# Performance work log

Hardware: AMD Instinct MI355X
Metric: run time of the kernel (lower is better)

The kernel has to match this reference:

```python
import jax, jax.numpy as jnp
import numpy as np

NUM_ITEMS = 50000
B = 512      # batch of (user, item) pairs
L = 50       # padded per-user item-list length
K = 20       # top_k: length of each context channel
H = 32       # hidden_dim
D = 32       # output_dim


def setup_inputs() -> dict:
    key = jax.random.key(0)
    ks = jax.random.split(key, 8)
    ctx = jax.random.normal(ks[0], (NUM_ITEMS, 10, K), dtype=jnp.float32)
    item_idxs = jax.random.randint(ks[1], (B,), 0, NUM_ITEMS)
    user_items = jax.random.randint(ks[2], (B, L), 0, NUM_ITEMS)
    user_lens = jax.random.randint(ks[3], (B,), 1, L + 1)  # ragged lengths in [1, L]
    W1 = jax.random.normal(ks[4], (5, 1, H), dtype=jnp.float32) * 0.1
    b1 = jnp.zeros((5, H), dtype=jnp.float32)
    W2 = jax.random.normal(ks[5], (5, H, D), dtype=jnp.float32) * 0.1
    b2 = jnp.zeros((5, D), dtype=jnp.float32)
    Wout = jax.random.normal(ks[6], (D, 1), dtype=jnp.float32) * 0.1
    bout = jnp.zeros((1,), dtype=jnp.float32)
    return dict(ctx=ctx, W1=W1, b1=b1, W2=W2, b2=b2, Wout=Wout, bout=bout,
                item_idxs=item_idxs, user_items=user_items, user_lens=user_lens)


def _item_rep(feat, W1, b1, W2, b2):
    """feat: [..., 10, K] context channels -> [..., 5*K, D] item representation.
    Channels (2c, 2c+1) go through com_{c+1}: a shared 1->H->D MLP applied to each
    scalar (unsqueeze(1) in the original), outputs of the two channels multiplied."""
    prefix = feat.shape[:-2]
    x = feat.reshape(prefix + (5, 2, K))                     # [..., 5, 2, K]
    w1 = W1[:, 0, :].reshape((5, 1, 1, H))                   # input_dim == 1
    h = jax.nn.relu(x[..., None] * w1 + b1.reshape((5, 1, 1, H)))   # [..., 5, 2, K, H]
    o = jnp.einsum('...cpkh,chd->...cpkd', h, W2) + b2.reshape((5, 1, 1, D))
    rep = o[..., 0, :, :] * o[..., 1, :, :]                  # [..., 5, K, D]
    return rep.reshape(prefix + (5 * K, D))


def reference(ctx, W1, b1, W2, b2, Wout, bout, item_idxs, user_items, user_lens):
    # Target-item representations: gather contexts then tiny MLPs. [B, 5K, D]
    item_rep = _item_rep(ctx[item_idxs], W1, b1, W2, b2)
    # Per-user item reps (padded ragged) and masked mean over the item list.
    u_rep = _item_rep(ctx[user_items], W1, b1, W2, b2)       # [B, L, 5K, D]
    mask = (jnp.arange(L)[None, :] < user_lens[:, None]).astype(u_rep.dtype)  # [B, L]
    u_mean = jnp.einsum('blnd,bl->bnd', u_rep, mask) / user_lens[:, None, None].astype(u_rep.dtype)
    inter = u_mean * item_rep                                # [B, 5K, D]
    pred = jax.nn.sigmoid(inter @ Wout + bout)               # [B, 5K, 1]
    return pred.reshape(B * 5 * K, 1)
```

## Files before the change

### kernel.cpp

```cpp
#include <hip/hip_runtime.h>
#include <math.h>

#define NITEMS 50000
#define BATCH  512
#define LLEN   50
#define KTOP   20
#define HDIM   32
#define DDIM   32
#define NCH    5
#define NSEG   33
#define NSCAL  200
#define NCELL  100
#define NCELLH 50
#define THRP   33
#define NWAVE  8
#define CSLOTH 7

typedef _Float16 h2 __attribute__((ext_vector_type(2)));

static __device__ __forceinline__ float dot2_acc(h2 a, h2 b, float c) {
#if __has_builtin(__builtin_amdgcn_fdot2)
    return __builtin_amdgcn_fdot2(a, b, c, false);
#else
    return fmaf((float)a.x, (float)b.x, fmaf((float)a.y, (float)b.y, c));
#endif
}

#define WS_THRS  0
#define WS_AB16  160
#define WS_ORDER 5440


__global__ __launch_bounds__(256) void cnn_setup(
        const float* __restrict__ W1, const float* __restrict__ b1,
        const float* __restrict__ W2, const float* __restrict__ b2,
        const int* __restrict__ user_lens,
        float* __restrict__ ws, int* __restrict__ order) {
    const int tid = threadIdx.x;

    if (blockIdx.x < NSEG) {
        __shared__ float sW1[NCH*HDIM], sB1[NCH*HDIM], sThr[NCH*HDIM];
        __shared__ int   sRank[NCH*HDIM];
        __shared__ float sW2[NCH*HDIM*DDIM];
        __shared__ float sB2[NCH*DDIM];

        for (int i = tid; i < NCH*HDIM; i += 256) { sW1[i] = W1[i]; sB1[i] = b1[i]; }
        for (int i = tid; i < NCH*HDIM*DDIM; i += 256) sW2[i] = W2[i];
        for (int i = tid; i < NCH*DDIM; i += 256) sB2[i] = b2[i];
        __syncthreads();

        for (int i = tid; i < NCH*HDIM; i += 256) {
            float w = sW1[i];
            sThr[i] = (w != 0.f) ? (-sB1[i] / w) : INFINITY;
        }
        __syncthreads();

        for (int i = tid; i < NCH*HDIM; i += 256) {
            int c = i / HDIM, h = i % HDIM;
            float thr = sThr[i];
            int rank = 0;
            for (int h2i = 0; h2i < HDIM; ++h2i) {
                float thr2 = sThr[c*HDIM + h2i];
                rank += (thr2 < thr || (thr2 == thr && h2i < h)) ? 1 : 0;
            }
            sRank[i] = rank;
            if (blockIdx.x == 0) ws[WS_THRS + c*HDIM + rank] = thr;
        }
        __syncthreads();

        const int s = blockIdx.x;
        if (tid < NCH*DDIM) {
            int c = tid / DDIM, d = tid % DDIM;
            float A = 0.f, Bv = 0.f;
#pragma unroll
            for (int h = 0; h < HDIM; ++h) {
                float w  = sW1[c*HDIM + h];
                float bb = sB1[c*HDIM + h];
                int   r  = sRank[c*HDIM + h];
                bool active = (w > 0.f) ? (r < s) : ((w < 0.f) ? (r >= s) : (bb > 0.f));
                if (active) {
                    float w2 = sW2[(c*HDIM + h)*DDIM + d];
                    A  = fmaf(w,  w2, A);
                    Bv = fmaf(bb, w2, Bv);
                }
            }
            Bv += sB2[c*DDIM + d];
            unsigned short* ab = (unsigned short*)(ws + WS_AB16);
            int d4 = d >> 2, dd = d & 3;
            int base = ((c*NSEG + s)*32 + d4*4)*2;
            _Float16 ah = (_Float16)A, bh = (_Float16)Bv;
            ab[base + 4*(dd>>1) + (dd&1)]     = __builtin_bit_cast(unsigned short, ah);
            ab[base + 4*(dd>>1) + 2 + (dd&1)] = __builtin_bit_cast(unsigned short, bh);
        }
    } else {
        __shared__ int sHist[LLEN + 1];
        for (int i = tid; i <= LLEN; i += 256) sHist[i] = 0;
        __syncthreads();
        for (int i = tid; i < BATCH; i += 256) atomicAdd(&sHist[user_lens[i]], 1);
        __syncthreads();
        if (tid == 0) {
            int accum = 0;
            for (int l = 1; l <= LLEN; ++l) { int c = sHist[l]; sHist[l] = accum; accum += c; }
        }
        __syncthreads();
        for (int i = tid; i < BATCH; i += 256) {
            int pos = atomicAdd(&sHist[user_lens[i]], 1);
            order[pos] = i;
        }
    }
}

__global__ __launch_bounds__(512, 8) void cnn_main(
        const float* __restrict__ ctx,  const float* __restrict__ ws,
        const float* __restrict__ Wout, const float* __restrict__ bout,
        const int* __restrict__ item_idxs, const int* __restrict__ user_items,
        const int* __restrict__ user_lens, const int* __restrict__ order,
        float* __restrict__ out) {
    __shared__ unsigned int sAB16[NCH*NSEG*32];
    __shared__ float  sThrS[NCH*THRP];
    __shared__ uint2  sxo[NWAVE][NCELLH];
    __shared__ uint2  sWt[NCELLH*8];
    __shared__ float  pRed[NWAVE][NCELLH];

    const int tid  = threadIdx.x;
    const int w    = tid >> 6;
    const int lane = tid & 63;
    const int g    = lane >> 3;
    const int d4   = lane & 7;

    const uint4* ABg = reinterpret_cast<const uint4*>(ws + WS_AB16);
    uint4* sAB4 = reinterpret_cast<uint4*>(sAB16);
    for (int i = tid; i < NCH*NSEG*8; i += 512) sAB4[i] = ABg[i];
    for (int i = tid; i < NCH*THRP; i += 512) {
        int c = i / THRP, j = i - c*THRP;
        sThrS[i] = (j < HDIM) ? ws[WS_THRS + c*HDIM + j] : 0.f;
    }

    const int rowSlot = blockIdx.x >> 1;
    const int half    = blockIdx.x & 1;
    const int rank = (rowSlot < 256) ? rowSlot : (767 - rowSlot);
    const int b    = order[rank];
    const int len  = user_lens[b];
    const float inv_len = 1.f / (float)len;
    const float bo = bout[0];
    const h2 wv0 = {(_Float16)Wout[4*d4],     (_Float16)Wout[4*d4 + 1]};
    const h2 wv1 = {(_Float16)Wout[4*d4 + 2], (_Float16)Wout[4*d4 + 3]};

    int sc[2], sdst[2], sgi[2];
#pragma unroll
    for (int r = 0; r < 2; ++r) {
        int lidx = lane + 64*r;
        int c    = lidx / 20, rr = lidx - c*20;
        int slot = rr / 10,  kk = rr - slot*10;
        sc[r]   = (lidx < 100) ? c : 0;
        sdst[r] = (c*10 + kk)*8 + slot*4;
        sgi[r]  = c*40 + slot*20 + half*10 + kk;
    }

    const int nstripe = (len > w) ? ((len - w + NWAVE - 1) / NWAVE) : 0;

    unsigned int wtA[CSLOTH], wtB[CSLOTH];
    float acc[CSLOTH];
#pragma unroll
    for (int i = 0; i < CSLOTH; ++i) acc[i] = 0.f;

    char* sxoB = (char*)&sxo[w][0];

    __syncthreads();

    float xp[2] = {0.f, 0.f};
    if (nstripe > 0) {
        const float* row = ctx + (size_t)user_items[b*LLEN + w] * NSCAL;
#pragma unroll
        for (int r = 0; r < 2; ++r) {
            int lidx = lane + 64*r;
            if (lidx < 100) xp[r] = row[sgi[r]];
        }
    }

    if (w == 0) {
        float xt[2] = {0.f, 0.f};
        const float* row = ctx + (size_t)item_idxs[b] * NSCAL;
#pragma unroll
        for (int r = 0; r < 2; ++r) {
            int lidx = lane + 64*r;
            if (lidx < 100) xt[r] = row[sgi[r]];
        }
#pragma unroll
        for (int r = 0; r < 2; ++r) {
            int lidx = lane + 64*r;
            if (lidx < 100) {
                float xv = xt[r];
                int base = sc[r]*THRP;
                int pos = 0;
                pos += (sThrS[base + pos + 15] < xv) ? 16 : 0;
                pos += (sThrS[base + pos + 7]  < xv) ? 8  : 0;
                pos += (sThrS[base + pos + 3]  < xv) ? 4  : 0;
                pos += (sThrS[base + pos + 1]  < xv) ? 2  : 0;
                pos += (sThrS[base + pos]      < xv) ? 1  : 0;
                unsigned int off = (unsigned int)((sc[r]*NSEG + pos) << 7);
                _Float16 xh = (_Float16)xv;
                unsigned int word = (unsigned int)__builtin_bit_cast(unsigned short, xh)
                                  | (off << 16);
                *(unsigned int*)(sxoB + sdst[r]) = word;
            }
        }
        __builtin_amdgcn_wave_barrier();
#pragma unroll
        for (int i = 0; i < CSLOTH; ++i) {
            int cell = g + 8*i;
            if (cell < NCELLH) {
                uint2 xo = sxo[0][cell];
                const uint4* p0 = (const uint4*)((const char*)sAB16 + (xo.x >> 16) + (d4 << 4));
                const uint4* p1 = (const uint4*)((const char*)sAB16 + (xo.y >> 16) + (d4 << 4));
                uint4 q0 = *p0, q1 = *p1;
                _Float16 x0h = __builtin_bit_cast(_Float16, (unsigned short)(xo.x & 0xffffu));
                _Float16 x1h = __builtin_bit_cast(_Float16, (unsigned short)(xo.y & 0xffffu));
                h2 x0 = {x0h, x0h}, x1 = {x1h, x1h};
                h2 repa = (x0 * __builtin_bit_cast(h2, q0.x) + __builtin_bit_cast(h2, q0.y))
                        * (x1 * __builtin_bit_cast(h2, q1.x) + __builtin_bit_cast(h2, q1.y));
                h2 repb = (x0 * __builtin_bit_cast(h2, q0.z) + __builtin_bit_cast(h2, q0.w))
                        * (x1 * __builtin_bit_cast(h2, q1.z) + __builtin_bit_cast(h2, q1.w));
                wtA[i] = __builtin_bit_cast(unsigned int, (h2)(repa * wv0));
                wtB[i] = __builtin_bit_cast(unsigned int, (h2)(repb * wv1));
                sWt[cell*8 + d4] = make_uint2(wtA[i], wtB[i]);
            }
        }
    }
    __syncthreads();

    if (w != 0) {
#pragma unroll
        for (int i = 0; i < CSLOTH; ++i) {
            int cell = g + 8*i;
            if (cell < NCELLH) {
                uint2 v = sWt[cell*8 + d4];
                wtA[i] = v.x; wtB[i] = v.y;
            }
        }
    }

    for (int j = 0; j < nstripe; ++j) {
        float xc[2];
#pragma unroll
        for (int r = 0; r < 2; ++r) xc[r] = xp[r];

        if (j + 1 < nstripe) {
            const float* row = ctx + (size_t)user_items[b*LLEN + w + NWAVE*(j+1)] * NSCAL;
#pragma unroll
            for (int r = 0; r < 2; ++r) {
                int lidx = lane + 64*r;
                if (lidx < 100) xp[r] = row[sgi[r]];
            }
        }

#pragma unroll
        for (int r = 0; r < 2; ++r) {
            int lidx = lane + 64*r;
            if (lidx < 100) {
                float xv = xc[r];
                int base = sc[r]*THRP;
                int pos = 0;
                pos += (sThrS[base + pos + 15] < xv) ? 16 : 0;
                pos += (sThrS[base + pos + 7]  < xv) ? 8  : 0;
                pos += (sThrS[base + pos + 3]  < xv) ? 4  : 0;
                pos += (sThrS[base + pos + 1]  < xv) ? 2  : 0;
                pos += (sThrS[base + pos]      < xv) ? 1  : 0;
                unsigned int off = (unsigned int)((sc[r]*NSEG + pos) << 7);
                _Float16 xh = (_Float16)xv;
                unsigned int word = (unsigned int)__builtin_bit_cast(unsigned short, xh)
                                  | (off << 16);
                *(unsigned int*)(sxoB + sdst[r]) = word;
            }
        }
        __builtin_amdgcn_wave_barrier();

#pragma unroll
        for (int i = 0; i < CSLOTH; ++i) {
            int cell = g + 8*i;
            if (cell < NCELLH) {
                uint2 xo = sxo[w][cell];
                const uint4* p0 = (const uint4*)((const char*)sAB16 + (xo.x >> 16) + (d4 << 4));
                const uint4* p1 = (const uint4*)((const char*)sAB16 + (xo.y >> 16) + (d4 << 4));
                uint4 q0 = *p0, q1 = *p1;
                _Float16 x0h = __builtin_bit_cast(_Float16, (unsigned short)(xo.x & 0xffffu));
                _Float16 x1h = __builtin_bit_cast(_Float16, (unsigned short)(xo.y & 0xffffu));
                h2 x0 = {x0h, x0h}, x1 = {x1h, x1h};
                h2 repa = (x0 * __builtin_bit_cast(h2, q0.x) + __builtin_bit_cast(h2, q0.y))
                        * (x1 * __builtin_bit_cast(h2, q1.x) + __builtin_bit_cast(h2, q1.y));
                h2 repb = (x0 * __builtin_bit_cast(h2, q0.z) + __builtin_bit_cast(h2, q0.w))
                        * (x1 * __builtin_bit_cast(h2, q1.z) + __builtin_bit_cast(h2, q1.w));
                acc[i] = dot2_acc(repa, __builtin_bit_cast(h2, wtA[i]),
                         dot2_acc(repb, __builtin_bit_cast(h2, wtB[i]), acc[i]));
            }
        }
        __builtin_amdgcn_wave_barrier();
    }

#pragma unroll
    for (int i = 0; i < CSLOTH; ++i) {
        int cell = g + 8*i;
        float v = acc[i];
        v += __shfl_xor(v, 1, 64);
        v += __shfl_xor(v, 2, 64);
        v += __shfl_xor(v, 4, 64);
        if (d4 == 0 && cell < NCELLH) pRed[w][cell] = v;
    }
    __syncthreads();
    if (tid < NCELLH) {
        float p = 0.f;
#pragma unroll
        for (int q = 0; q < NWAVE; ++q) p += pRed[q][tid];
        int cellG = (tid / 10)*KTOP + half*10 + (tid % 10);
        out[b*NCELL + cellG] = 1.f / (1.f + expf(-(p*inv_len + bo)));
    }
}

extern "C" void kernel_launch(void* const* d_in, const int* in_sizes, int n_in,
                              void* d_out, int out_size, void* d_ws, size_t ws_size,
                              hipStream_t stream) {
    const float* ctx   = (const float*)d_in[0];
    const float* W1    = (const float*)d_in[1];
    const float* b1    = (const float*)d_in[2];
    const float* W2    = (const float*)d_in[3];
    const float* b2    = (const float*)d_in[4];
    const float* Wout  = (const float*)d_in[5];
    const float* bout  = (const float*)d_in[6];
    const int* item_idxs  = (const int*)d_in[7];
    const int* user_items = (const int*)d_in[8];
    const int* user_lens  = (const int*)d_in[9];
    float* out = (float*)d_out;
    float* ws  = (float*)d_ws;
    int*   order = (int*)(ws + WS_ORDER);

    cnn_setup<<<NSEG + 1, 256, 0, stream>>>(W1, b1, W2, b2, user_lens, ws, order);
    cnn_main<<<2*BATCH, 512, 0, stream>>>(ctx, ws, Wout, bout,
                                          item_idxs, user_items, user_lens,
                                          order, out);
}
```

Baseline: 112.9 us.

## Compute segment tables with prefix sums in one block; read two cell slots from global

The setup kernel now builds all 33 piecewise-linear segment coefficient tables in a single block. It walks the sorted thresholds once with running prefix sums instead of launching one block per segment that each redo the full masked reduction. In the main loop, cell slots 4 and 5 now load their A/B coefficient quads straight from the global workspace rather than from LDS, to spread the load traffic across the L1 and LDS paths. The incremental sums can round differently from the direct per-segment sums, and the global loads add memory latency inside the hot loop.

```diff
diff --git a/kernel.cpp b/kernel.cpp
--- a/kernel.cpp
+++ b/kernel.cpp
@@ -26,6 +26,19 @@
 #endif
 }
 
+static __device__ __forceinline__ float cellterm(uint2 xo, uint4 q0, uint4 q1,
+        unsigned int wa, unsigned int wb, float a) {
+    _Float16 x0h = __builtin_bit_cast(_Float16, (unsigned short)(xo.x & 0xffffu));
+    _Float16 x1h = __builtin_bit_cast(_Float16, (unsigned short)(xo.y & 0xffffu));
+    h2 x0 = {x0h, x0h}, x1 = {x1h, x1h};
+    h2 repa = (x0 * __builtin_bit_cast(h2, q0.x) + __builtin_bit_cast(h2, q0.y))
+            * (x1 * __builtin_bit_cast(h2, q1.x) + __builtin_bit_cast(h2, q1.y));
+    h2 repb = (x0 * __builtin_bit_cast(h2, q0.z) + __builtin_bit_cast(h2, q0.w))
+            * (x1 * __builtin_bit_cast(h2, q1.z) + __builtin_bit_cast(h2, q1.w));
+    return dot2_acc(repa, __builtin_bit_cast(h2, wa),
+           dot2_acc(repb, __builtin_bit_cast(h2, wb), a));
+}
+
 #define WS_THRS  0
 #define WS_AB16  160
 #define WS_ORDER 5440
@@ -38,9 +51,9 @@
         float* __restrict__ ws, int* __restrict__ order) {
     const int tid = threadIdx.x;
 
-    if (blockIdx.x < NSEG) {
+    if (blockIdx.x == 0) {
         __shared__ float sW1[NCH*HDIM], sB1[NCH*HDIM], sThr[NCH*HDIM];
-        __shared__ int   sRank[NCH*HDIM];
+        __shared__ int   sInv[NCH*HDIM];
         __shared__ float sW2[NCH*HDIM*DDIM];
         __shared__ float sB2[NCH*DDIM];
 
@@ -63,34 +76,52 @@
                 float thr2 = sThr[c*HDIM + h2i];
                 rank += (thr2 < thr || (thr2 == thr && h2i < h)) ? 1 : 0;
             }
-            sRank[i] = rank;
-            if (blockIdx.x == 0) ws[WS_THRS + c*HDIM + rank] = thr;
-        }
-        __syncthreads();
-
-        const int s = blockIdx.x;
+            sInv[c*HDIM + rank] = h;
+            ws[WS_THRS + c*HDIM + rank] = thr;
+        }
+        __syncthreads();
+
         if (tid < NCH*DDIM) {
-            int c = tid / DDIM, d = tid % DDIM;
-            float A = 0.f, Bv = 0.f;
+            const int c = tid >> 5, d = tid & 31;
+            const int cb = c << 5;
+            float sa = 0.f, sb = 0.f, zb = 0.f;
 #pragma unroll
             for (int h = 0; h < HDIM; ++h) {
-                float w  = sW1[c*HDIM + h];
-                float bb = sB1[c*HDIM + h];
-                int   r  = sRank[c*HDIM + h];
-                bool active = (w > 0.f) ? (r < s) : ((w < 0.f) ? (r >= s) : (bb > 0.f));
-                if (active) {
-                    float w2 = sW2[(c*HDIM + h)*DDIM + d];
-                    A  = fmaf(w,  w2, A);
-                    Bv = fmaf(bb, w2, Bv);
+                float wv = sW1[cb + h];
+                float bb = sB1[cb + h];
+                float w2 = sW2[((cb + h) << 5) + d];
+                float aw = wv * w2, bw = bb * w2;
+                if (wv < 0.f) { sa += aw; sb += bw; }
+                else if (wv == 0.f && bb > 0.f) zb += bw;
+            }
+            const float b2v = sB2[cb + d] + zb;
+            unsigned int pk[NSEG];
+            float pa = 0.f, pb = 0.f;
+#pragma unroll
+            for (int s = 0; s < NSEG; ++s) {
+                _Float16 ah = (_Float16)(pa + sa);
+                _Float16 bh = (_Float16)(pb + sb + b2v);
+                pk[s] = (unsigned int)__builtin_bit_cast(unsigned short, ah)
+                      | ((unsigned int)__builtin_bit_cast(unsigned short, bh) << 16);
+                if (s < HDIM) {
+                    int hh = sInv[cb + s];
+                    float wv = sW1[cb + hh];
+                    float bb = sB1[cb + hh];
+                    float w2 = sW2[((cb + hh) << 5) + d];
+                    float aw = wv * w2, bw = bb * w2;
+                    if (wv > 0.f)      { pa += aw; pb += bw; }
+                    else if (wv < 0.f) { sa -= aw; sb -= bw; }
                 }
             }
-            Bv += sB2[c*DDIM + d];
             unsigned short* ab = (unsigned short*)(ws + WS_AB16);
-            int d4 = d >> 2, dd = d & 3;
-            int base = ((c*NSEG + s)*32 + d4*4)*2;
-            _Float16 ah = (_Float16)A, bh = (_Float16)Bv;
-            ab[base + 4*(dd>>1) + (dd&1)]     = __builtin_bit_cast(unsigned short, ah);
-            ab[base + 4*(dd>>1) + 2 + (dd&1)] = __builtin_bit_cast(unsigned short, bh);
+            const int dq = d >> 2, dd = d & 3;
+            const int sub = 4*(dd>>1) + (dd&1);
+#pragma unroll
+            for (int s = 0; s < NSEG; ++s) {
+                int base = ((c*NSEG + s)*32 + dq*4)*2;
+                ab[base + sub]     = (unsigned short)(pk[s] & 0xffffu);
+                ab[base + sub + 2] = (unsigned short)(pk[s] >> 16);
+            }
         }
     } else {
         __shared__ int sHist[LLEN + 1];
@@ -128,9 +159,11 @@
     const int g    = lane >> 3;
     const int d4   = lane & 7;
 
-    const uint4* ABg = reinterpret_cast<const uint4*>(ws + WS_AB16);
+    const char* ABg = (const char*)(ws + WS_AB16);
+
+    const uint4* ABv = reinterpret_cast<const uint4*>(ws + WS_AB16);
     uint4* sAB4 = reinterpret_cast<uint4*>(sAB16);
-    for (int i = tid; i < NCH*NSEG*8; i += 512) sAB4[i] = ABg[i];
+    for (int i = tid; i < NCH*NSEG*8; i += 512) sAB4[i] = ABv[i];
     for (int i = tid; i < NCH*THRP; i += 512) {
         int c = i / THRP, j = i - c*THRP;
         sThrS[i] = (j < HDIM) ? ws[WS_THRS + c*HDIM + j] : 0.f;
@@ -211,9 +244,8 @@
             int cell = g + 8*i;
             if (cell < NCELLH) {
                 uint2 xo = sxo[0][cell];
-                const uint4* p0 = (const uint4*)((const char*)sAB16 + (xo.x >> 16) + (d4 << 4));
-                const uint4* p1 = (const uint4*)((const char*)sAB16 + (xo.y >> 16) + (d4 << 4));
-                uint4 q0 = *p0, q1 = *p1;
+                uint4 q0 = *(const uint4*)((const char*)sAB16 + (xo.x >> 16) + (d4 << 4));
+                uint4 q1 = *(const uint4*)((const char*)sAB16 + (xo.y >> 16) + (d4 << 4));
                 _Float16 x0h = __builtin_bit_cast(_Float16, (unsigned short)(xo.x & 0xffffu));
                 _Float16 x1h = __builtin_bit_cast(_Float16, (unsigned short)(xo.y & 0xffffu));
                 h2 x0 = {x0h, x0h}, x1 = {x1h, x1h};
@@ -275,25 +307,25 @@
         }
         __builtin_amdgcn_wave_barrier();
 
+        uint2 xo4 = sxo[w][g + 32];
+        uint2 xo5 = sxo[w][g + 40];
+        uint4 q40 = *(const uint4*)(ABg + (xo4.x >> 16) + (d4 << 4));
+        uint4 q41 = *(const uint4*)(ABg + (xo4.y >> 16) + (d4 << 4));
+        uint4 q50 = *(const uint4*)(ABg + (xo5.x >> 16) + (d4 << 4));
+        uint4 q51 = *(const uint4*)(ABg + (xo5.y >> 16) + (d4 << 4));
 #pragma unroll
         for (int i = 0; i < CSLOTH; ++i) {
+            if (i == 4 || i == 5) continue;
             int cell = g + 8*i;
             if (cell < NCELLH) {
                 uint2 xo = sxo[w][cell];
-                const uint4* p0 = (const uint4*)((const char*)sAB16 + (xo.x >> 16) + (d4 << 4));
-                const uint4* p1 = (const uint4*)((const char*)sAB16 + (xo.y >> 16) + (d4 << 4));
-                uint4 q0 = *p0, q1 = *p1;
-                _Float16 x0h = __builtin_bit_cast(_Float16, (unsigned short)(xo.x & 0xffffu));
-                _Float16 x1h = __builtin_bit_cast(_Float16, (unsigned short)(xo.y & 0xffffu));
-                h2 x0 = {x0h, x0h}, x1 = {x1h, x1h};
-                h2 repa = (x0 * __builtin_bit_cast(h2, q0.x) + __builtin_bit_cast(h2, q0.y))
-                        * (x1 * __builtin_bit_cast(h2, q1.x) + __builtin_bit_cast(h2, q1.y));
-                h2 repb = (x0 * __builtin_bit_cast(h2, q0.z) + __builtin_bit_cast(h2, q0.w))
-                        * (x1 * __builtin_bit_cast(h2, q1.z) + __builtin_bit_cast(h2, q1.w));
-                acc[i] = dot2_acc(repa, __builtin_bit_cast(h2, wtA[i]),
-                         dot2_acc(repb, __builtin_bit_cast(h2, wtB[i]), acc[i]));
-            }
-        }
+                uint4 q0 = *(const uint4*)((const char*)sAB16 + (xo.x >> 16) + (d4 << 4));
+                uint4 q1 = *(const uint4*)((const char*)sAB16 + (xo.y >> 16) + (d4 << 4));
+                acc[i] = cellterm(xo, q0, q1, wtA[i], wtB[i], acc[i]);
+            }
+        }
+        acc[4] = cellterm(xo4, q40, q41, wtA[4], wtB[4], acc[4]);
+        acc[5] = cellterm(xo5, q50, q51, wtA[5], wtB[5], acc[5]);
         __builtin_amdgcn_wave_barrier();
     }
 
@@ -333,7 +365,7 @@
     float* ws  = (float*)d_ws;
     int*   order = (int*)(ws + WS_ORDER);
 
-    cnn_setup<<<NSEG + 1, 256, 0, stream>>>(W1, b1, W2, b2, user_lens, ws, order);
+    cnn_setup<<<2, 256, 0, stream>>>(W1, b1, W2, b2, user_lens, ws, order);
     cnn_main<<<2*BATCH, 512, 0, stream>>>(ctx, ws, Wout, bout,
                                           item_idxs, user_items, user_lens,
                                           order, out);
```

Measured after the change: 171.9 us. 1.52x slower.
